# Kernel optimization log

Measured on AMD Instinct MI355X. Metric: run time of the kernel, lower is better.

The kernel has to match this reference:

```python
import jax, jax.numpy as jnp
import numpy as np

EMBED = 1024
HEADS = 16
HEAD_DIM = EMBED // HEADS


def setup_inputs() -> dict:
    key = jax.random.key(0)
    ks = jax.random.split(key, 11)
    N, S = 2, 2048
    scale = 1.0 / np.sqrt(EMBED)
    inp = {
        "values": jax.random.normal(ks[0], (N, S, EMBED), jnp.float32),
        "keys": jax.random.normal(ks[1], (N, S, EMBED), jnp.float32),
        "queries": jax.random.normal(ks[2], (N, S, EMBED), jnp.float32),
        "W_v": jax.random.normal(ks[3], (EMBED, EMBED), jnp.float32) * scale,
        "b_v": jnp.zeros((EMBED,), jnp.float32),
        "W_k": jax.random.normal(ks[4], (EMBED, EMBED), jnp.float32) * scale,
        "b_k": jnp.zeros((EMBED,), jnp.float32),
        "W_q": jax.random.normal(ks[5], (EMBED, EMBED), jnp.float32) * scale,
        "b_q": jnp.zeros((EMBED,), jnp.float32),
        "W_o": jax.random.normal(ks[6], (EMBED, EMBED), jnp.float32) * scale,
        "b_o": jnp.zeros((EMBED,), jnp.float32),
    }
    return inp


def reference(values, keys, queries, W_v, b_v, W_k, b_k, W_q, b_q, W_o, b_o):
    N, q_len, _ = queries.shape
    # linear projections then split heads: [N, S, H, Dh]
    v = (values @ W_v.T + b_v).reshape(N, -1, HEADS, HEAD_DIM)
    k = (keys @ W_k.T + b_k).reshape(N, -1, HEADS, HEAD_DIM)
    q = (queries @ W_q.T + b_q).reshape(N, q_len, HEADS, HEAD_DIM)
    # raw scores [N, H, Q, K]
    energy = jnp.einsum("nqhd,nkhd->nhqk", q, k)
    attention = jax.nn.softmax(energy / np.sqrt(HEAD_DIM), axis=-1)
    out = jnp.einsum("nhql,nlhd->nqhd", attention, v).reshape(N, q_len, EMBED)
    return out @ W_o.T + b_o
```

## Files before the change

### kernel.cpp

```cpp
#include <hip/hip_runtime.h>
#include <hip/hip_bf16.h>


typedef short bf16x8 __attribute__((ext_vector_type(8)));
typedef short bf16x4 __attribute__((ext_vector_type(4)));
typedef float f32x4 __attribute__((ext_vector_type(4)));
typedef float f32x16 __attribute__((ext_vector_type(16)));
typedef unsigned u32x2 __attribute__((ext_vector_type(2)));
typedef unsigned u32x4 __attribute__((ext_vector_type(4)));

constexpr int S = 2048;
constexpr int E = 1024;
constexpr int H = 16;
constexpr int D = 64;
constexpr int M = 2 * S;
#define QSCALE 0.18033688011112042f

static __device__ __forceinline__ short f2bf_rne(float x) {
  unsigned u = __builtin_bit_cast(unsigned, x);
  u += 0x7fff + ((u >> 16) & 1);
  return (short)(u >> 16);
}
static __device__ __forceinline__ bf16x8 cvt8(float4 a, float4 b) {
  bf16x8 t;
  t[0] = f2bf_rne(a.x); t[1] = f2bf_rne(a.y);
  t[2] = f2bf_rne(a.z); t[3] = f2bf_rne(a.w);
  t[4] = f2bf_rne(b.x); t[5] = f2bf_rne(b.y);
  t[6] = f2bf_rne(b.z); t[7] = f2bf_rne(b.w);
  return t;
}
static __device__ __forceinline__ float fast_exp2(float x) {
#if __has_builtin(__builtin_amdgcn_exp2f)
  return __builtin_amdgcn_exp2f(x);
#else
  return __expf(0.69314718055994531f * x);
#endif
}
static __device__ __forceinline__ unsigned cvtpk(float a, float b) {
  unsigned r;
  asm("v_cvt_pk_bf16_f32 %0, %1, %2" : "=v"(r) : "v"(a), "v"(b));
  return r;
}
static __device__ __forceinline__ void plswap(unsigned& a, unsigned& b) {
#if __has_builtin(__builtin_amdgcn_permlane32_swap)
  u32x2 t = __builtin_amdgcn_permlane32_swap(a, b, false, false);
  a = t[0]; b = t[1];
#else
  asm("v_permlane32_swap_b32 %0, %1" : "+v"(a), "+v"(b));
#endif
}
static __device__ __forceinline__ void lds_barrier() {
  asm volatile("s_waitcnt lgkmcnt(0)" ::: "memory");
  __builtin_amdgcn_s_barrier();
}

static __device__ __forceinline__ void gl_lds16(const short* g, short* l) {
  __builtin_amdgcn_global_load_lds(
      (const __attribute__((address_space(1))) void*)g,
      (__attribute__((address_space(3))) void*)l, 16, 0, 0);
}


__global__ __launch_bounds__(256) void cast_all(
    const float* __restrict__ qs, const float* __restrict__ ks,
    const float* __restrict__ vsrc, const float* __restrict__ wq,
    const float* __restrict__ wk, const float* __restrict__ wv,
    const float* __restrict__ wo, short* __restrict__ qbf,
    short* __restrict__ kbf, short* __restrict__ vbf, short* __restrict__ wqb,
    short* __restrict__ wkb, short* __restrict__ wvb, short* __restrict__ wob) {
  const float* s;
  short* d;
  switch (blockIdx.y) {
    case 0: s = qs; d = qbf; break;
    case 1: s = ks; d = kbf; break;
    case 2: s = vsrc; d = vbf; break;
    case 3: if (blockIdx.x >= 512) return; s = wq; d = wqb; break;
    case 4: if (blockIdx.x >= 512) return; s = wk; d = wkb; break;
    case 5: if (blockIdx.x >= 512) return; s = wv; d = wvb; break;
    default: if (blockIdx.x >= 512) return; s = wo; d = wob; break;
  }
  size_t i = ((size_t)blockIdx.x * 256 + threadIdx.x) * 8;
  *(bf16x8*)&d[i] = cvt8(*(const float4*)&s[i], *(const float4*)&s[i + 4]);
}

__global__ __launch_bounds__(256) void qk_gemm(
    const short* __restrict__ qbf, const short* __restrict__ kbf,
    const short* __restrict__ wqb, const short* __restrict__ wkb,
    const float* __restrict__ bq, const float* __restrict__ bk,
    short* __restrict__ qb, short* __restrict__ kb) {
  __shared__ __align__(16) short as[128 * 32];
  __shared__ __align__(16) short bs[128 * 32];
  const int tid = threadIdx.x;
  const int lane = tid & 63, w = tid >> 6;
  const int l15 = lane & 15, quad = lane >> 4;
  const int wm = w & 1, wn = w >> 1;

  const int b = blockIdx.x;
  const int c = b & 7, r = b >> 3;
  const int bn = r & 7;
  const int t = c * 8 + (r >> 3);
  const int z = t >> 5, bm = t & 31;

  const short* A = z ? kbf : qbf;
  const short* Bw = z ? wkb : wqb;
  const float* bias = z ? bk : bq;

  const short* agp[2];
  const short* bgp[2];
  int ldsb[2];
#pragma unroll
  for (int cc = 0; cc < 2; ++cc) {
    int seg = w * 2 + cc;
    int p = seg * 8 + (lane >> 3), kc = lane & 7;
    int l = kc ^ (p & 7);
    int row = 2 * p + (l >> 2), col = (l & 3) * 8;
    ldsb[cc] = seg * 512;
    agp[cc] = &A[(size_t)(bm * 128 + row) * E + col];
    bgp[cc] = &Bw[(size_t)(bn * 128 + row) * E + col];
  }

  f32x4 acc[4][4] = {};
  for (int k0 = 0; k0 < E; k0 += 32) {
    __syncthreads();
#pragma unroll
    for (int cc = 0; cc < 2; ++cc) {
      gl_lds16(agp[cc] + k0, &as[ldsb[cc]]);
      gl_lds16(bgp[cc] + k0, &bs[ldsb[cc]]);
    }
    __syncthreads();

    bf16x8 af[4], bf[4];
#pragma unroll
    for (int tt = 0; tt < 4; ++tt) {
      int ra = wm * 64 + tt * 16 + l15;
      int pa2 = ra >> 1, la = (ra & 1) * 4 + quad, ka = la ^ (pa2 & 7);
      af[tt] = *(bf16x8*)&as[pa2 * 64 + ka * 8];
      int rb = wn * 64 + tt * 16 + l15;
      int pb2 = rb >> 1, lb = (rb & 1) * 4 + quad, kb2 = lb ^ (pb2 & 7);
      bf[tt] = *(bf16x8*)&bs[pb2 * 64 + kb2 * 8];
    }
#pragma unroll
    for (int mt = 0; mt < 4; ++mt)
#pragma unroll
      for (int nt = 0; nt < 4; ++nt)
        acc[mt][nt] = __builtin_amdgcn_mfma_f32_16x16x32_bf16(
            af[mt], bf[nt], acc[mt][nt], 0, 0, 0);
  }

#pragma unroll
  for (int mt = 0; mt < 4; ++mt)
#pragma unroll
    for (int nt = 0; nt < 4; ++nt)
#pragma unroll
      for (int rr = 0; rr < 4; ++rr) {
        int row = bm * 128 + wm * 64 + mt * 16 + quad * 4 + rr;
        int col = bn * 128 + wn * 64 + nt * 16 + l15;
        float v = acc[mt][nt][rr] + bias[col];
        int n = row >> 11, s = row & 2047, h = col >> 6, d = col & 63;
        if (z == 0) {
          qb[(((size_t)(n * H + h) * S) + s) * D + d] = f2bf_rne(v * QSCALE);
        } else {
          kb[(((size_t)(n * H + h) * S) + s) * D + d] = f2bf_rne(v);
        }
      }
}

template <int MODE>
__global__ __launch_bounds__(256) void gemm64(const short* __restrict__ A,
                                              const short* __restrict__ Bw,
                                              const float* __restrict__ bias,
                                              void* __restrict__ outp) {
  __shared__ __align__(16) short as[64 * 32];
  __shared__ __align__(16) short bs[128 * 32];
  const int tid = threadIdx.x;
  const int lane = tid & 63, w = tid >> 6;
  const int l15 = lane & 15, quad = lane >> 4;
  const int wm = w & 1, wn = w >> 1;

  const int b = blockIdx.x;
  const int c = b & 7, r = b >> 3;
  const int bn = r & 7;
  const int bm = c * 8 + (r >> 3);

  const short* agp;
  int aldsb;
  {
    int seg = w;
    int p = seg * 8 + (lane >> 3), kc = lane & 7;
    int l = kc ^ (p & 7);
    int row = 2 * p + (l >> 2), col = (l & 3) * 8;
    aldsb = seg * 512;
    agp = &A[(size_t)(bm * 64 + row) * E + col];
  }
  const short* bgp[2];
  int bldsb[2];
#pragma unroll
  for (int cc = 0; cc < 2; ++cc) {
    int seg = w * 2 + cc;
    int p = seg * 8 + (lane >> 3), kc = lane & 7;
    int l = kc ^ (p & 7);
    int row = 2 * p + (l >> 2), col = (l & 3) * 8;
    bldsb[cc] = seg * 512;
    bgp[cc] = &Bw[(size_t)(bn * 128 + row) * E + col];
  }

  f32x4 acc[2][4] = {};
  for (int k0 = 0; k0 < E; k0 += 32) {
    __syncthreads();
    gl_lds16(agp + k0, &as[aldsb]);
#pragma unroll
    for (int cc = 0; cc < 2; ++cc) gl_lds16(bgp[cc] + k0, &bs[bldsb[cc]]);
    __syncthreads();

    bf16x8 af[2], bf[4];
#pragma unroll
    for (int tt = 0; tt < 2; ++tt) {
      int ra = wm * 32 + tt * 16 + l15;
      int pa2 = ra >> 1, la = (ra & 1) * 4 + quad, ka = la ^ (pa2 & 7);
      af[tt] = *(bf16x8*)&as[pa2 * 64 + ka * 8];
    }
#pragma unroll
    for (int tt = 0; tt < 4; ++tt) {
      int rb = wn * 64 + tt * 16 + l15;
      int pb2 = rb >> 1, lb = (rb & 1) * 4 + quad, kb2 = lb ^ (pb2 & 7);
      bf[tt] = *(bf16x8*)&bs[pb2 * 64 + kb2 * 8];
    }
#pragma unroll
    for (int mt = 0; mt < 2; ++mt)
#pragma unroll
      for (int nt = 0; nt < 4; ++nt)
        acc[mt][nt] = __builtin_amdgcn_mfma_f32_16x16x32_bf16(
            af[mt], bf[nt], acc[mt][nt], 0, 0, 0);
  }

#pragma unroll
  for (int mt = 0; mt < 2; ++mt)
#pragma unroll
    for (int nt = 0; nt < 4; ++nt)
#pragma unroll
      for (int rr = 0; rr < 4; ++rr) {
        int row = bm * 64 + wm * 32 + mt * 16 + quad * 4 + rr;
        int col = bn * 128 + wn * 64 + nt * 16 + l15;
        float v = acc[mt][nt][rr] + bias[col];
        if (MODE == 0) {
          int n = row >> 11, s = row & 2047, h = col >> 6, d = col & 63;
          ((short*)outp)[(((size_t)(n * H + h) * D) + d) * S + s] =
              f2bf_rne(v);
        } else {
          ((float*)outp)[(size_t)row * E + col] = v;
        }
      }
}

__global__ __launch_bounds__(512) void attn_kernel(const short* __restrict__ q,
                                                   const short* __restrict__ k,
                                                   const short* __restrict__ vt,
                                                   short* __restrict__ ctx) {
  __shared__ __align__(16) short ksb[2][128 * 72];
  __shared__ __align__(16) short vsb[2][64 * 136];

  const int tid = threadIdx.x;
  const int lane = tid & 63, wv = tid >> 6;
  const int l31 = lane & 31, h = lane >> 5;

  const int bid = blockIdx.y * gridDim.x + blockIdx.x;
  const int c = bid & 7, r = bid >> 3;
  const int qt = r & 7;
  const int hz = c * 4 + (r >> 3);
  const int hh = hz & 15, nn = hz >> 4;

  const size_t base = (size_t)(nn * H + hh) * S * D;
  const int q0 = qt * 256 + wv * 32;

  bf16x8 qf[4];
#pragma unroll
  for (int kd = 0; kd < 4; ++kd)
    qf[kd] = *(const bf16x8*)&q[base + (size_t)(q0 + l31) * D + kd * 16 + h * 8];

  f32x16 o[2] = {};
  float lsum = 0.f;

  bf16x8 pk[2], pv[2];
  auto loadKV = [&](int j0) {
#pragma unroll
    for (int cc = 0; cc < 2; ++cc) {
      int ch = cc * 512 + tid;
      int kr = ch >> 3, kc = (ch & 7) * 8;
      pk[cc] = *(const bf16x8*)&k[base + (size_t)(j0 + kr) * D + kc];
      int vr = ch >> 4, vc = (ch & 15) * 8;
      pv[cc] = *(const bf16x8*)&vt[base + (size_t)vr * S + j0 + vc];
    }
  };
  auto storeKV = [&](int bufi) {
#pragma unroll
    for (int cc = 0; cc < 2; ++cc) {
      int ch = cc * 512 + tid;
      int kr = ch >> 3, kc = (ch & 7) * 8;
      *(bf16x8*)&ksb[bufi][kr * 72 + kc] = pk[cc];
      int vr = ch >> 4, vc = (ch & 15) * 8;
      *(bf16x8*)&vsb[bufi][vr * 136 + vc] = pv[cc];
    }
  };

  loadKV(0);
  storeKV(0);
  loadKV(128);
  lds_barrier();

  for (int t = 0; t < 16; ++t) {
    const int cur = t & 1;
    if (t + 1 < 16) storeKV(cur ^ 1);
    if (t + 2 < 16) loadKV((t + 2) * 128);
    const short* ks = ksb[cur];
    const short* vs = vsb[cur];

#pragma unroll
    for (int half = 0; half < 2; ++half) {
      f32x16 sc[2] = {};
      __builtin_amdgcn_s_setprio(1);
#pragma unroll
      for (int c2 = 0; c2 < 2; ++c2)
#pragma unroll
        for (int kd = 0; kd < 4; ++kd) {
          bf16x8 kf = *(bf16x8*)&ks[(half * 64 + c2 * 32 + l31) * 72 +
                                    kd * 16 + h * 8];
          sc[c2] = __builtin_amdgcn_mfma_f32_32x32x16_bf16(kf, qf[kd], sc[c2],
                                                           0, 0, 0);
        }
      __builtin_amdgcn_s_setprio(0);

      bf16x8 pa[4];
#pragma unroll
      for (int c2 = 0; c2 < 2; ++c2) {
        float pe[16];
#pragma unroll
        for (int rr = 0; rr < 16; ++rr) {
          float p = fast_exp2(sc[c2][rr]);
          lsum += p;
          pe[rr] = p;
        }
#pragma unroll
        for (int kk = 0; kk < 2; ++kk) {
          unsigned A0 = cvtpk(pe[8 * kk + 0], pe[8 * kk + 1]);
          unsigned A1 = cvtpk(pe[8 * kk + 2], pe[8 * kk + 3]);
          unsigned B0 = cvtpk(pe[8 * kk + 4], pe[8 * kk + 5]);
          unsigned B1 = cvtpk(pe[8 * kk + 6], pe[8 * kk + 7]);
          plswap(A0, B0);
          plswap(A1, B1);
          u32x4 tt;
          tt[0] = A0; tt[1] = A1; tt[2] = B0; tt[3] = B1;
          pa[c2 * 2 + kk] = __builtin_bit_cast(bf16x8, tt);
        }
      }

      __builtin_amdgcn_s_setprio(1);
#pragma unroll
      for (int ks2 = 0; ks2 < 4; ++ks2)
#pragma unroll
        for (int dc = 0; dc < 2; ++dc) {
          bf16x8 vf = *(bf16x8*)&vs[(dc * 32 + l31) * 136 + half * 64 +
                                    ks2 * 16 + h * 8];
          o[dc] = __builtin_amdgcn_mfma_f32_32x32x16_bf16(pa[ks2], vf, o[dc],
                                                          0, 0, 0);
        }
      __builtin_amdgcn_s_setprio(0);
    }
    lds_barrier();
  }

  lsum += __shfl_xor(lsum, 32);
  float invq = 1.0f / lsum;

#pragma unroll
  for (int rr = 0; rr < 16; ++rr) {
    int crow = (rr & 3) + 8 * (rr >> 2) + 4 * h;
    float inv = __shfl(invq, crow);
    int row = q0 + crow;
#pragma unroll
    for (int dc = 0; dc < 2; ++dc) {
      ctx[((size_t)(nn * S + row)) * E + hh * D + dc * 32 + l31] =
          f2bf_rne(o[dc][rr] * inv);
    }
  }
}

extern "C" void kernel_launch(void* const* d_in, const int* in_sizes, int n_in,
                              void* d_out, int out_size, void* d_ws,
                              size_t ws_size, hipStream_t stream) {
  const float* values  = (const float*)d_in[0];
  const float* keys    = (const float*)d_in[1];
  const float* queries = (const float*)d_in[2];
  const float* b_v = (const float*)d_in[4];
  const float* b_k = (const float*)d_in[6];
  const float* b_q = (const float*)d_in[8];
  const float* W_v = (const float*)d_in[3];
  const float* W_k = (const float*)d_in[5];
  const float* W_q = (const float*)d_in[7];
  const float* W_o = (const float*)d_in[9];
  const float* b_o = (const float*)d_in[10];

  const size_t X = (size_t)M * E;
  const size_t W = (size_t)E * E;

  short* qbf = (short*)d_out;
  short* qb  = (short*)d_out + X;
  short* kbf = (short*)d_ws;
  short* vbf = kbf + X;
  short* vtb = vbf + X;
  short* wqb = vtb + X;
  short* wkb = wqb + W;
  short* wvb = wkb + W;
  short* wob = wvb + W;
  short* ctx = kbf;
  short* kb  = vbf;

  cast_all<<<dim3(2048, 7), 256, 0, stream>>>(queries, keys, values, W_q, W_k,
                                              W_v, W_o, qbf, kbf, vbf, wqb,
                                              wkb, wvb, wob);
  gemm64<0><<<512, 256, 0, stream>>>(vbf, wvb, b_v, vtb);
  qk_gemm<<<512, 256, 0, stream>>>(qbf, kbf, wqb, wkb, b_q, b_k, qb, kb);
  attn_kernel<<<dim3(8, 32), 512, 0, stream>>>(qb, kb, vtb, ctx);
  gemm64<1><<<512, 256, 0, stream>>>(ctx, wob, b_o, d_out);
}
```

Before: 210.1 us.

## Fuse activation fp32-to-bf16 cast into merged QKV projection GEMM

Drops the separate cast pass over the three fp32 activation tensors. The projection GEMM now reads fp32 activations directly into registers, converts them to bf16, and writes them to LDS, with the next k-tile's loads issued early as a prefetch. Q, K and V projections are merged into one 768-block launch, so V no longer needs its own GEMM launch and writes its transposed layout directly. In exchange, A-tile reads double in bytes and go through registers instead of direct global-to-LDS loads, which adds VGPR pressure and conversion work inside the main loop.

```diff
diff --git a/kernel.cpp b/kernel.cpp
--- a/kernel.cpp
+++ b/kernel.cpp
@@ -61,33 +61,30 @@
 }
 
 
-__global__ __launch_bounds__(256) void cast_all(
-    const float* __restrict__ qs, const float* __restrict__ ks,
-    const float* __restrict__ vsrc, const float* __restrict__ wq,
-    const float* __restrict__ wk, const float* __restrict__ wv,
-    const float* __restrict__ wo, short* __restrict__ qbf,
-    short* __restrict__ kbf, short* __restrict__ vbf, short* __restrict__ wqb,
-    short* __restrict__ wkb, short* __restrict__ wvb, short* __restrict__ wob) {
+__global__ __launch_bounds__(256) void cast_w(
+    const float* __restrict__ wq, const float* __restrict__ wk,
+    const float* __restrict__ wv, const float* __restrict__ wo,
+    short* __restrict__ wqb, short* __restrict__ wkb,
+    short* __restrict__ wvb, short* __restrict__ wob) {
   const float* s;
   short* d;
   switch (blockIdx.y) {
-    case 0: s = qs; d = qbf; break;
-    case 1: s = ks; d = kbf; break;
-    case 2: s = vsrc; d = vbf; break;
-    case 3: if (blockIdx.x >= 512) return; s = wq; d = wqb; break;
-    case 4: if (blockIdx.x >= 512) return; s = wk; d = wkb; break;
-    case 5: if (blockIdx.x >= 512) return; s = wv; d = wvb; break;
-    default: if (blockIdx.x >= 512) return; s = wo; d = wob; break;
+    case 0: s = wq; d = wqb; break;
+    case 1: s = wk; d = wkb; break;
+    case 2: s = wv; d = wvb; break;
+    default: s = wo; d = wob; break;
   }
   size_t i = ((size_t)blockIdx.x * 256 + threadIdx.x) * 8;
   *(bf16x8*)&d[i] = cvt8(*(const float4*)&s[i], *(const float4*)&s[i + 4]);
 }
 
-__global__ __launch_bounds__(256) void qk_gemm(
-    const short* __restrict__ qbf, const short* __restrict__ kbf,
-    const short* __restrict__ wqb, const short* __restrict__ wkb,
+__global__ __launch_bounds__(256) void proj_gemm(
+    const float* __restrict__ qs, const float* __restrict__ ks,
+    const float* __restrict__ vsrc, const short* __restrict__ wqb,
+    const short* __restrict__ wkb, const short* __restrict__ wvb,
     const float* __restrict__ bq, const float* __restrict__ bk,
-    short* __restrict__ qb, short* __restrict__ kb) {
+    const float* __restrict__ bv, short* __restrict__ qb,
+    short* __restrict__ kb, short* __restrict__ vtb) {
   __shared__ __align__(16) short as[128 * 32];
   __shared__ __align__(16) short bs[128 * 32];
   const int tid = threadIdx.x;
@@ -98,14 +95,14 @@
   const int b = blockIdx.x;
   const int c = b & 7, r = b >> 3;
   const int bn = r & 7;
-  const int t = c * 8 + (r >> 3);
+  const int t = c * 12 + (r >> 3);
   const int z = t >> 5, bm = t & 31;
 
-  const short* A = z ? kbf : qbf;
-  const short* Bw = z ? wkb : wqb;
-  const float* bias = z ? bk : bq;
-
-  const short* agp[2];
+  const float* A = z == 0 ? qs : (z == 1 ? ks : vsrc);
+  const short* Bw = z == 0 ? wqb : (z == 1 ? wkb : wvb);
+  const float* bias = z == 0 ? bq : (z == 1 ? bk : bv);
+
+  const float* afp[2];
   const short* bgp[2];
   int ldsb[2];
 #pragma unroll
@@ -115,19 +112,35 @@
     int l = kc ^ (p & 7);
     int row = 2 * p + (l >> 2), col = (l & 3) * 8;
     ldsb[cc] = seg * 512;
-    agp[cc] = &A[(size_t)(bm * 128 + row) * E + col];
+    afp[cc] = &A[(size_t)(bm * 128 + row) * E + col];
     bgp[cc] = &Bw[(size_t)(bn * 128 + row) * E + col];
   }
 
+  float4 ar[2][2];
+  auto loadA = [&](int k0) {
+#pragma unroll
+    for (int cc = 0; cc < 2; ++cc) {
+      ar[cc][0] = *(const float4*)(afp[cc] + k0);
+      ar[cc][1] = *(const float4*)(afp[cc] + k0 + 4);
+    }
+  };
+
+  loadA(0);
   f32x4 acc[4][4] = {};
   for (int k0 = 0; k0 < E; k0 += 32) {
+    lds_barrier();
+#pragma unroll
+    for (int cc = 0; cc < 2; ++cc) {
+      u32x4 pck;
+      pck[0] = cvtpk(ar[cc][0].x, ar[cc][0].y);
+      pck[1] = cvtpk(ar[cc][0].z, ar[cc][0].w);
+      pck[2] = cvtpk(ar[cc][1].x, ar[cc][1].y);
+      pck[3] = cvtpk(ar[cc][1].z, ar[cc][1].w);
+      *(u32x4*)&as[ldsb[cc] + lane * 8] = pck;
+      gl_lds16(bgp[cc] + k0, &bs[ldsb[cc]]);
+    }
     __syncthreads();
-#pragma unroll
-    for (int cc = 0; cc < 2; ++cc) {
-      gl_lds16(agp[cc] + k0, &as[ldsb[cc]]);
-      gl_lds16(bgp[cc] + k0, &bs[ldsb[cc]]);
-    }
-    __syncthreads();
+    if (k0 + 32 < E) loadA(k0 + 32);
 
     bf16x8 af[4], bf[4];
 #pragma unroll
@@ -159,8 +172,10 @@
         int n = row >> 11, s = row & 2047, h = col >> 6, d = col & 63;
         if (z == 0) {
           qb[(((size_t)(n * H + h) * S) + s) * D + d] = f2bf_rne(v * QSCALE);
+        } else if (z == 1) {
+          kb[(((size_t)(n * H + h) * S) + s) * D + d] = f2bf_rne(v);
         } else {
-          kb[(((size_t)(n * H + h) * S) + s) * D + d] = f2bf_rne(v);
+          vtb[(((size_t)(n * H + h) * D) + d) * S + s] = f2bf_rne(v);
         }
       }
 }
@@ -402,23 +417,19 @@
   const size_t X = (size_t)M * E;
   const size_t W = (size_t)E * E;
 
-  short* qbf = (short*)d_out;
-  short* qb  = (short*)d_out + X;
-  short* kbf = (short*)d_ws;
-  short* vbf = kbf + X;
-  short* vtb = vbf + X;
-  short* wqb = vtb + X;
+  short* qb = (short*)d_out;
+  short* kb = (short*)d_out + X;
+  short* vtb = (short*)d_ws;
+  short* ctx = vtb + X;
+  short* wqb = ctx + X;
   short* wkb = wqb + W;
   short* wvb = wkb + W;
   short* wob = wvb + W;
-  short* ctx = kbf;
-  short* kb  = vbf;
-
-  cast_all<<<dim3(2048, 7), 256, 0, stream>>>(queries, keys, values, W_q, W_k,
-                                              W_v, W_o, qbf, kbf, vbf, wqb,
-                                              wkb, wvb, wob);
-  gemm64<0><<<512, 256, 0, stream>>>(vbf, wvb, b_v, vtb);
-  qk_gemm<<<512, 256, 0, stream>>>(qbf, kbf, wqb, wkb, b_q, b_k, qb, kb);
+
+  cast_w<<<dim3(512, 4), 256, 0, stream>>>(W_q, W_k, W_v, W_o,
+                                           wqb, wkb, wvb, wob);
+  proj_gemm<<<768, 256, 0, stream>>>(queries, keys, values, wqb, wkb, wvb,
+                                     b_q, b_k, b_v, qb, kb, vtb);
   attn_kernel<<<dim3(8, 32), 512, 0, stream>>>(qb, kb, vtb, ctx);
   gemm64<1><<<512, 256, 0, stream>>>(ctx, wob, b_o, d_out);
 }
```

Result: slower. 221.2 us (+5.3%).
